# Kernel tuning notes

Measured on AMD Instinct MI355X. Metric: run time of the kernel, lower is better.

The kernel has to match this reference:

```python
import jax, jax.numpy as jnp
import numpy as np

N = 50000          # nodes
E = 1600000        # edges (avg degree 32)
G = 256            # graphs in batch
IN_DIM = 128
HID = 64
NUM_LAYERS = 12    # stacked layers after the first
NUM_REL = 3
NEG_SLOPE = 0.2    # RGATConv default leaky_relu slope


def setup_inputs() -> dict:
    key = jax.random.key(0)
    ks = jax.random.split(key, 12)
    return {
        "node_features": jax.random.normal(ks[0], (N, IN_DIM), jnp.float32),
        "edge_index": jax.random.randint(ks[1], (2, E), 0, N, jnp.int32),
        "edge_type": jax.random.randint(ks[2], (E,), 0, NUM_REL, jnp.int32),
        "batch_index": jnp.sort(jax.random.randint(ks[3], (N,), 0, G, jnp.int32)),
        "W_first": jax.random.normal(ks[4], (NUM_REL, IN_DIM, HID), jnp.float32) / np.sqrt(IN_DIM).astype(np.float32),
        "q_first": jax.random.normal(ks[5], (HID,), jnp.float32) / np.sqrt(HID).astype(np.float32),
        "k_first": jax.random.normal(ks[6], (HID,), jnp.float32) / np.sqrt(HID).astype(np.float32),
        "b_first": jnp.zeros((HID,), jnp.float32),
        "W_stack": jax.random.normal(ks[7], (NUM_LAYERS, NUM_REL, HID, HID), jnp.float32) / np.sqrt(HID).astype(np.float32),
        "q_stack": jax.random.normal(ks[8], (NUM_LAYERS, HID), jnp.float32) / np.sqrt(HID).astype(np.float32),
        "k_stack": jax.random.normal(ks[9], (NUM_LAYERS, HID), jnp.float32) / np.sqrt(HID).astype(np.float32),
        "b_stack": jnp.zeros((NUM_LAYERS, HID), jnp.float32),
        "t": jnp.ones((1,), jnp.float32),
    }


def _segment_softmax(logits, seg, num_segments):
    # numerically-stable softmax over entries sharing a segment id (PyG `softmax`)
    m = jax.ops.segment_max(logits, seg, num_segments=num_segments)
    m = jnp.where(jnp.isfinite(m), m, 0.0)  # empty segments -> -inf, neutralize
    e = jnp.exp(logits - m[seg])
    s = jax.ops.segment_sum(e, seg, num_segments=num_segments)
    return e / (s[seg] + 1e-16)


def _rgat_layer(x, W, q, k, b, src, dst, etype):
    # PyG RGATConv, heads=1, dim=1, additive-self-attention, across-relation softmax.
    n = x.shape[0]
    xr = jnp.einsum('ni,rio->rno', x, W)       # [R,N,H] per-relation transform of all nodes
    qn = jnp.einsum('rno,o->rn', xr, q)        # [R,N] query scalar (out_i @ q)
    kn = jnp.einsum('rno,o->rn', xr, k)        # [R,N] key scalar   (out_j @ k)
    logits = jax.nn.leaky_relu(qn[etype, dst] + kn[etype, src], NEG_SLOPE)  # [E]
    alpha = _segment_softmax(logits, dst, n)   # softmax over incoming edges of each dst
    msg = alpha[:, None] * xr[etype, src]      # [E,H]
    return jax.ops.segment_sum(msg, dst, num_segments=n) + b


def reference(node_features, edge_index, edge_type, batch_index,
              W_first, q_first, k_first, b_first,
              W_stack, q_stack, k_stack, b_stack, t):
    src, dst = edge_index[0], edge_index[1]   # PyG convention: row=source j, col=target i
    x1 = _rgat_layer(node_features, W_first, q_first, k_first, b_first, src, dst, edge_type)

    def step(x, p):
        W, q, k, b = p
        y = _rgat_layer(x, W, q, k, b, src, dst, edge_type)
        return y, y

    _, ys = jax.lax.scan(step, x1, (W_stack, q_stack, k_stack, b_stack))
    all_x = jnp.concatenate([x1[None], ys], axis=0)                 # [13,N,H]
    node_rep = jnp.transpose(all_x, (1, 0, 2)).reshape(node_features.shape[0], -1)  # [N,13*H]

    # SoftmaxAggregation(learn=True): per-feature softmax over nodes of each graph
    alpha_g = _segment_softmax(node_rep * t[0], batch_index, G)     # [N,13*H]
    graph_rep = jax.ops.segment_sum(node_rep * alpha_g, batch_index, num_segments=G)
    return graph_rep, node_rep
```

## Files before the change

### kernel.cpp

```cpp
#include <hip/hip_runtime.h>
#include <math.h>

#define NN 50000
#define NE 1600000
#define NG 256
#define IND 128
#define HID 64
#define NREL 3
#define SLOPE 0.2f
#define XRS 192
#define NRS 832
#define WTP 136
#define W0SZ (192*128)
#define WLSZ (192*64)
#define WTOT (W0SZ + 12*WLSZ)

typedef short bf16x8 __attribute__((ext_vector_type(8)));
typedef float f32x4 __attribute__((ext_vector_type(4)));

__device__ __forceinline__ float wred_max(float v){
  #pragma unroll
  for (int o = 32; o; o >>= 1) v = fmaxf(v, __shfl_xor(v, o));
  return v;
}
__device__ __forceinline__ float wred_sum(float v){
  #pragma unroll
  for (int o = 32; o; o >>= 1) v += __shfl_xor(v, o);
  return v;
}

__device__ __forceinline__ unsigned short f2bf(float f){
  unsigned int u = __float_as_uint(f);
  u = (u + 0x7FFFu + ((u >> 16) & 1u)) >> 16;
  return (unsigned short)u;
}
__device__ __forceinline__ float bf2f(unsigned short h){
  return __uint_as_float(((unsigned int)h) << 16);
}


__global__ void hist_kernel(const int* __restrict__ dst, int* __restrict__ cnts){
  int e = blockIdx.x * blockDim.x + threadIdx.x;
  if (e < NE) atomicAdd(&cnts[dst[e]], 1);
}

__global__ void scan1_kernel(const int* __restrict__ cnts, int* __restrict__ rowp,
                             int* __restrict__ bsum){
  __shared__ int ws[16];
  int b = blockIdx.x, tid = threadIdx.x;
  int i = b * 1024 + tid;
  int lane = tid & 63, wid = tid >> 6;
  int v = (i < NN) ? cnts[i] : 0;
  int x = v;
  #pragma unroll
  for (int o = 1; o < 64; o <<= 1){ int t = __shfl_up(x, o); if (lane >= o) x += t; }
  if (lane == 63) ws[wid] = x;
  __syncthreads();
  if (tid < 16){
    int y = ws[tid];
    #pragma unroll
    for (int o = 1; o < 16; o <<= 1){ int t = __shfl_up(y, o); if (tid >= o) y += t; }
    ws[tid] = y;
  }
  __syncthreads();
  int off = (wid > 0) ? ws[wid - 1] : 0;
  x += off;
  if (i < NN) rowp[i] = x - v;
  if (tid == 1023) bsum[b] = x;
}

__global__ void scan2_kernel(int* __restrict__ bsum, int* __restrict__ rowp, int nb){
  int tid = threadIdx.x;
  int v = (tid < nb) ? bsum[tid] : 0;
  int x = v;
  #pragma unroll
  for (int o = 1; o < 64; o <<= 1){ int t = __shfl_up(x, o); if (tid >= o) x += t; }
  if (tid < nb) bsum[tid] = x - v;
  if (tid == 63) rowp[NN] = x;
}

__global__ void scan3_kernel(int* __restrict__ rowp, const int* __restrict__ bsum){
  int i = blockIdx.x * 1024 + threadIdx.x;
  if (i < NN) rowp[i] += bsum[blockIdx.x];
}

__global__ void scatter_kernel(const int* __restrict__ src, const int* __restrict__ dst,
                               const int* __restrict__ et, const int* __restrict__ rowp,
                               int* __restrict__ fill, int* __restrict__ csr){
  int e = blockIdx.x * blockDim.x + threadIdx.x;
  if (e >= NE) return;
  int d = dst[e];
  int pos = atomicAdd(&fill[d], 1);
  csr[rowp[d] + pos] = src[e] | (et[e] << 24);
}

__global__ void gstart_kernel(const int* __restrict__ batch, int* __restrict__ gst){
  int n = blockIdx.x * blockDim.x + threadIdx.x;
  if (n > NN) return;
  int bc = (n < NN) ? batch[n] : NG;
  int bp = (n == 0) ? -1 : batch[n - 1];
  for (int g = bp + 1; g <= bc; ++g) gst[g] = n;
}

__global__ void wprep13_kernel(const float* __restrict__ Wf, const float* __restrict__ Ws,
                               unsigned short* __restrict__ Wtg13){
  int i = blockIdx.x * blockDim.x + threadIdx.x;
  if (i >= WTOT) return;
  int j, K; size_t base; const float* W;
  if (i < W0SZ){ j = i; K = IND; base = 0; W = Wf; }
  else {
    int t = i - W0SZ;
    int l = t / WLSZ;
    j = t - l * WLSZ; K = HID;
    base = W0SZ + (size_t)l * WLSZ;
    W = Ws + (size_t)l * WLSZ;
  }
  int h = j & 63;
  int k = (j >> 6) % K;
  int r = j / (K * HID);
  Wtg13[base + (size_t)((r << 6) + h) * K + k] = f2bf(W[j]);
}

__global__ __launch_bounds__(256) void mm_kernel(
    const float* __restrict__ x, int ldx, int K,
    const unsigned short* __restrict__ Wtg,
    const float* __restrict__ qv, const float* __restrict__ kv,
    unsigned short* __restrict__ XRb, float* __restrict__ QK){
  __shared__ unsigned short Wt[192 * WTP];
  int tid = threadIdx.x;
  int w = tid >> 6, lane = tid & 63;
  int lrow = lane & 15, kg = lane >> 4;
  int row0 = blockIdx.x * 64;
  int row = row0 + w * 16 + lrow;
  int nb8 = 192 * (K >> 3);
  for (int i = tid; i < nb8; i += 256){
    int col = i / (K >> 3);
    int k8 = (i - col * (K >> 3)) << 3;
    *(bf16x8*)&Wt[col * WTP + k8] = *(const bf16x8*)&Wtg[(size_t)col * K + k8];
  }
  __syncthreads();

  f32x4 acc[12];
  #pragma unroll
  for (int t = 0; t < 12; ++t) acc[t] = (f32x4){0.f, 0.f, 0.f, 0.f};

  int ksteps = K >> 5;
  for (int ks = 0; ks < ksteps; ++ks){
    bf16x8 xb;
    if (row < NN){
      const float* xp = x + (size_t)row * ldx + (ks << 5) + (kg << 3);
      float4 v0 = *(const float4*)xp;
      float4 v1 = *(const float4*)(xp + 4);
      xb[0] = (short)f2bf(v0.x); xb[1] = (short)f2bf(v0.y);
      xb[2] = (short)f2bf(v0.z); xb[3] = (short)f2bf(v0.w);
      xb[4] = (short)f2bf(v1.x); xb[5] = (short)f2bf(v1.y);
      xb[6] = (short)f2bf(v1.z); xb[7] = (short)f2bf(v1.w);
    } else {
      #pragma unroll
      for (int j = 0; j < 8; ++j) xb[j] = 0;
    }
    int kk = (ks << 5) + (kg << 3);
    #pragma unroll
    for (int t = 0; t < 12; ++t){
      bf16x8 wf = *(const bf16x8*)&Wt[(t * 16 + lrow) * WTP + kk];
      acc[t] = __builtin_amdgcn_mfma_f32_16x16x32_bf16(wf, xb, acc[t], 0, 0, 0);
    }
  }

  if (row < NN){
    unsigned short* orow = XRb + (size_t)row * XRS;
    #pragma unroll
    for (int t = 0; t < 12; ++t){
      ushort4 o4;
      o4.x = f2bf(acc[t][0]); o4.y = f2bf(acc[t][1]);
      o4.z = f2bf(acc[t][2]); o4.w = f2bf(acc[t][3]);
      *(ushort4*)(orow + t * 16 + (kg << 2)) = o4;
    }
  }

  float pq[3] = {0,0,0}, pk[3] = {0,0,0};
  #pragma unroll
  for (int t = 0; t < 12; ++t){
    int r = t >> 2;
    int hbase = ((t & 3) << 4) + (kg << 2);
    #pragma unroll
    for (int j = 0; j < 4; ++j){
      float qc = qv[hbase + j], kc = kv[hbase + j];
      pq[r] = fmaf(acc[t][j], qc, pq[r]);
      pk[r] = fmaf(acc[t][j], kc, pk[r]);
    }
  }
  #pragma unroll
  for (int o = 16; o < 64; o <<= 1){
    #pragma unroll
    for (int r = 0; r < 3; ++r){
      pq[r] += __shfl_xor(pq[r], o);
      pk[r] += __shfl_xor(pk[r], o);
    }
  }
  if (kg == 0 && row < NN){
    #pragma unroll
    for (int r = 0; r < 3; ++r){
      QK[row * 8 + r] = pq[r];
      QK[row * 8 + 3 + r] = pk[r];
    }
  }
}


__global__ __launch_bounds__(256) void edge_kernel(
    const unsigned short* __restrict__ XRb, const float* __restrict__ QK,
    const int* __restrict__ csr, const int* __restrict__ rowp,
    const float* __restrict__ bias, float* __restrict__ out){
  int wid = blockIdx.x * 4 + (threadIdx.x >> 6);
  int lane = threadIdx.x & 63;
  if (wid >= NN) return;
  int beg = rowp[wid], end = rowp[wid + 1];
  int cnt = end - beg;
  float* orow = out + (size_t)wid * NRS;
  int sub = lane & 7;
  int g   = lane >> 3;
  if (cnt == 0){
    if (lane < 8){
      float4 b0 = *(const float4*)(bias + sub * 8);
      float4 b1 = *(const float4*)(bias + sub * 8 + 4);
      *(float4*)(orow + sub * 8) = b0;
      *(float4*)(orow + sub * 8 + 4) = b1;
    }
    return;
  }
  float q0 = QK[wid * 8], q1 = QK[wid * 8 + 1], q2 = QK[wid * 8 + 2];

  if (cnt <= 128){
    float l0 = -INFINITY, l1 = -INFINITY;
    int o0 = 0, o1 = 0;
    {
      int idx = beg + lane;
      if (idx < end){
        int pk = csr[idx];
        int sn = pk & 0xFFFFFF, et = pk >> 24;
        float lg = (et == 0 ? q0 : (et == 1 ? q1 : q2)) + QK[sn * 8 + 3 + et];
        l0 = lg >= 0.f ? lg : lg * SLOPE;
        o0 = sn * XRS + et * HID;
      }
      idx += 64;
      if (idx < end){
        int pk = csr[idx];
        int sn = pk & 0xFFFFFF, et = pk >> 24;
        float lg = (et == 0 ? q0 : (et == 1 ? q1 : q2)) + QK[sn * 8 + 3 + et];
        l1 = lg >= 0.f ? lg : lg * SLOPE;
        o1 = sn * XRS + et * HID;
      }
    }
    float m = wred_max(fmaxf(l0, l1));
    float e0 = __expf(l0 - m), e1 = __expf(l1 - m);
    float s = wred_sum(e0 + e1);
    float inv = 1.f / (s + 1e-16f);
    float w0 = e0 * inv, w1 = e1 * inv;

    const unsigned short* xp = XRb + sub * 8;
    float acc[8] = {};

    float wS[8]; int oS[8];
    #pragma unroll
    for (int e = 0; e < 8; ++e){
      int sl = (e << 3) + g;
      wS[e] = __shfl(w0, sl);
      oS[e] = __shfl(o0, sl);
    }
    int nIt = (min(cnt, 64) + 7) >> 3;
    #pragma unroll
    for (int e = 0; e < 8; ++e){
      uint4 d = *(const uint4*)(xp + oS[e]);
      float we = wS[e];
      acc[0] = fmaf(we, __uint_as_float(d.x << 16), acc[0]);
      acc[1] = fmaf(we, __uint_as_float(d.x & 0xFFFF0000u), acc[1]);
      acc[2] = fmaf(we, __uint_as_float(d.y << 16), acc[2]);
      acc[3] = fmaf(we, __uint_as_float(d.y & 0xFFFF0000u), acc[3]);
      acc[4] = fmaf(we, __uint_as_float(d.z << 16), acc[4]);
      acc[5] = fmaf(we, __uint_as_float(d.z & 0xFFFF0000u), acc[5]);
      acc[6] = fmaf(we, __uint_as_float(d.w << 16), acc[6]);
      acc[7] = fmaf(we, __uint_as_float(d.w & 0xFFFF0000u), acc[7]);
      if (e + 1 >= nIt) break;
    }
    if (cnt > 64){
      #pragma unroll
      for (int e = 0; e < 8; ++e){
        int sl = (e << 3) + g;
        wS[e] = __shfl(w1, sl);
        oS[e] = __shfl(o1, sl);
      }
      int nIt2 = (cnt - 64 + 7) >> 3;
      #pragma unroll
      for (int e = 0; e < 8; ++e){
        uint4 d = *(const uint4*)(xp + oS[e]);
        float we = wS[e];
        acc[0] = fmaf(we, __uint_as_float(d.x << 16), acc[0]);
        acc[1] = fmaf(we, __uint_as_float(d.x & 0xFFFF0000u), acc[1]);
        acc[2] = fmaf(we, __uint_as_float(d.y << 16), acc[2]);
        acc[3] = fmaf(we, __uint_as_float(d.y & 0xFFFF0000u), acc[3]);
        acc[4] = fmaf(we, __uint_as_float(d.z << 16), acc[4]);
        acc[5] = fmaf(we, __uint_as_float(d.z & 0xFFFF0000u), acc[5]);
        acc[6] = fmaf(we, __uint_as_float(d.w << 16), acc[6]);
        acc[7] = fmaf(we, __uint_as_float(d.w & 0xFFFF0000u), acc[7]);
        if (e + 1 >= nIt2) break;
      }
    }
    #pragma unroll
    for (int o = 8; o < 64; o <<= 1)
      #pragma unroll
      for (int j = 0; j < 8; ++j)
        acc[j] += __shfl_xor(acc[j], o);
    if (lane < 8){
      float4 b0 = *(const float4*)(bias + sub * 8);
      float4 b1 = *(const float4*)(bias + sub * 8 + 4);
      float4 r0, r1;
      r0.x = acc[0] + b0.x; r0.y = acc[1] + b0.y; r0.z = acc[2] + b0.z; r0.w = acc[3] + b0.w;
      r1.x = acc[4] + b1.x; r1.y = acc[5] + b1.y; r1.z = acc[6] + b1.z; r1.w = acc[7] + b1.w;
      *(float4*)(orow + sub * 8) = r0;
      *(float4*)(orow + sub * 8 + 4) = r1;
    }
    return;
  }

  float bv = bias[lane];
  float m = -INFINITY, s = 0.f;
  for (int c = beg; c < end; c += 64){
    int idx = c + lane;
    float l = -INFINITY;
    if (idx < end){
      int pk = csr[idx];
      int sn = pk & 0xFFFFFF, et = pk >> 24;
      float lg = (et == 0 ? q0 : (et == 1 ? q1 : q2)) + QK[sn * 8 + 3 + et];
      l = lg >= 0.f ? lg : lg * SLOPE;
    }
    float mnew = fmaxf(m, wred_max(l));
    float ps = wred_sum((idx < end) ? __expf(l - mnew) : 0.f);
    s = s * __expf(m - mnew) + ps;
    m = mnew;
  }
  float inv = 1.f / (s + 1e-16f);
  float acc = 0.f;
  for (int c = beg; c < end; c += 64){
    int idx = c + lane;
    int off = 0; float wgt = 0.f;
    if (idx < end){
      int pk = csr[idx];
      int sn = pk & 0xFFFFFF, et = pk >> 24;
      float lg = (et == 0 ? q0 : (et == 1 ? q1 : q2)) + QK[sn * 8 + 3 + et];
      float l = lg >= 0.f ? lg : lg * SLOPE;
      wgt = __expf(l - m) * inv;
      off = sn * XRS + et * HID;
    }
    int cc = min(64, end - c);
    #pragma unroll 4
    for (int j = 0; j < cc; ++j){
      float wj = __uint_as_float(__builtin_amdgcn_readlane(__float_as_uint(wgt), j));
      int oj = __builtin_amdgcn_readlane(off, j);
      acc = fmaf(wj, bf2f(XRb[oj + lane]), acc);
    }
  }
  orow[lane] = acc + bv;
}


__global__ __launch_bounds__(256) void agg_kernel(
    const float* __restrict__ nr, const int* __restrict__ gst,
    const float* __restrict__ tp, float* __restrict__ out){
  __shared__ float rm[4][64], rs[4][64], ra[4][64];
  int g = blockIdx.x;
  int lane = threadIdx.x & 63;
  int w = threadIdx.x >> 6;
  int f = blockIdx.y * 64 + lane;
  int s = gst[g], e = gst[g + 1];
  float tval = tp[0];
  float m = -INFINITY, ss = 0.f, ac = 0.f;
  for (int n = s + w; n < e; n += 4){
    float v = nr[(size_t)n * NRS + f];
    float vm = v * tval;
    float Mn = fmaxf(m, vm);
    float sc = __expf(m - Mn);
    float ev = __expf(vm - Mn);
    ss = ss * sc + ev;
    ac = ac * sc + v * ev;
    m = Mn;
  }
  rm[w][lane] = m; rs[w][lane] = ss; ra[w][lane] = ac;
  __syncthreads();
  if (w == 0){
    float M = fmaxf(fmaxf(rm[0][lane], rm[1][lane]), fmaxf(rm[2][lane], rm[3][lane]));
    float S = 0.f, A = 0.f;
    #pragma unroll
    for (int i = 0; i < 4; ++i){
      float si = rs[i][lane];
      float sci = (si > 0.f) ? __expf(rm[i][lane] - M) : 0.f;
      S = fmaf(si, sci, S);
      A = fmaf(ra[i][lane], sci, A);
    }
    out[(size_t)g * NRS + f] = A / (S + 1e-16f);
  }
}


extern "C" void kernel_launch(void* const* d_in, const int* in_sizes, int n_in,
                              void* d_out, int out_size, void* d_ws, size_t ws_size,
                              hipStream_t stream){
  const float* x0   = (const float*)d_in[0];
  const int*   eidx = (const int*)d_in[1];
  const int*   etyp = (const int*)d_in[2];
  const int*   batch= (const int*)d_in[3];
  const float* Wf   = (const float*)d_in[4];
  const float* qf   = (const float*)d_in[5];
  const float* kf   = (const float*)d_in[6];
  const float* bf   = (const float*)d_in[7];
  const float* Ws   = (const float*)d_in[8];
  const float* qs   = (const float*)d_in[9];
  const float* ks   = (const float*)d_in[10];
  const float* bs   = (const float*)d_in[11];
  const float* tp   = (const float*)d_in[12];

  float* gout = (float*)d_out;
  float* nrep = gout + (size_t)NG * NRS;

  char* w = (char*)d_ws;
  unsigned short* XRb = (unsigned short*)w; w += (size_t)NN * XRS * 2;
  float* QK   = (float*)w;  w += (size_t)NN * 8 * 4;
  unsigned short* Wtg13 = (unsigned short*)w; w += (size_t)WTOT * 2;
  int*   rowp = (int*)w;    w += (size_t)(NN + 2) * 4;
  int*   cnts = (int*)w;    w += (size_t)NN * 4;
  int*   gst  = (int*)w;    w += (size_t)(NG + 2) * 4;
  int*   bsum = (int*)w;    w += 64 * 4;
  int*   csr  = (int*)w;    w += (size_t)NE * 4;

  const int* srcv = eidx;
  const int* dstv = eidx + NE;

  const int NB = (NN + 1023) / 1024;

  hipMemsetAsync(cnts, 0, (size_t)NN * 4, stream);
  hist_kernel<<<(NE + 255) / 256, 256, 0, stream>>>(dstv, cnts);
  scan1_kernel<<<NB, 1024, 0, stream>>>(cnts, rowp, bsum);
  scan2_kernel<<<1, 64, 0, stream>>>(bsum, rowp, NB);
  scan3_kernel<<<NB, 1024, 0, stream>>>(rowp, bsum);
  hipMemsetAsync(cnts, 0, (size_t)NN * 4, stream);
  scatter_kernel<<<(NE + 255) / 256, 256, 0, stream>>>(srcv, dstv, etyp, rowp, cnts, csr);
  gstart_kernel<<<(NN + 256) / 256, 256, 0, stream>>>(batch, gst);
  wprep13_kernel<<<(WTOT + 255) / 256, 256, 0, stream>>>(Wf, Ws, Wtg13);

  for (int l = 0; l < 13; ++l){
    int K = (l == 0) ? IND : HID;
    const unsigned short* Wtg = Wtg13 + ((l == 0) ? 0 : (W0SZ + (size_t)(l - 1) * WLSZ));
    const float* q  = (l == 0) ? qf : (qs + (size_t)(l - 1) * HID);
    const float* kv = (l == 0) ? kf : (ks + (size_t)(l - 1) * HID);
    const float* b  = (l == 0) ? bf : (bs + (size_t)(l - 1) * HID);
    const float* x  = (l == 0) ? x0 : (nrep + (size_t)(l - 1) * HID);
    int ldx = (l == 0) ? IND : NRS;
    mm_kernel<<<(NN + 63) / 64, 256, 0, stream>>>(x, ldx, K, Wtg, q, kv, XRb, QK);
    edge_kernel<<<(NN + 3) / 4, 256, 0, stream>>>(XRb, QK, csr, rowp, b, nrep + (size_t)l * HID);
  }
  dim3 ag(NG, 13);
  agg_kernel<<<ag, 256, 0, stream>>>(nrep, gst, tp, gout);
}
```

Measured before the change: 1.016 ms.

## Build CSR via two-level bucket sort with shared-memory atomics

```diff
diff --git a/kernel.cpp b/kernel.cpp
--- a/kernel.cpp
+++ b/kernel.cpp
@@ -14,6 +14,8 @@
 #define W0SZ (192*128)
 #define WLSZ (192*64)
 #define WTOT (W0SZ + 12*WLSZ)
+#define NBKT 49
+#define ACHUNK 4096
 
 typedef short bf16x8 __attribute__((ext_vector_type(8)));
 typedef float f32x4 __attribute__((ext_vector_type(4)));
@@ -39,22 +41,76 @@
 }
 
 
-__global__ void hist_kernel(const int* __restrict__ dst, int* __restrict__ cnts){
-  int e = blockIdx.x * blockDim.x + threadIdx.x;
-  if (e < NE) atomicAdd(&cnts[dst[e]], 1);
-}
-
-__global__ void scan1_kernel(const int* __restrict__ cnts, int* __restrict__ rowp,
-                             int* __restrict__ bsum){
+__global__ __launch_bounds__(256) void bhistA_kernel(const int* __restrict__ dst,
+                                                     int* __restrict__ bkt_cnt){
+  __shared__ int h[64];
+  int tid = threadIdx.x;
+  if (tid < 64) h[tid] = 0;
+  __syncthreads();
+  int e0 = blockIdx.x * ACHUNK;
+  int e1 = min(e0 + ACHUNK, NE);
+  for (int i = e0 + tid; i < e1; i += 256)
+    atomicAdd(&h[dst[i] >> 10], 1);
+  __syncthreads();
+  if (tid < 64 && h[tid] > 0) atomicAdd(&bkt_cnt[tid], h[tid]);
+}
+
+__global__ void bscan_kernel(const int* __restrict__ bkt_cnt, int* __restrict__ bkt_base,
+                             int* __restrict__ bkt_fill, int* __restrict__ rowp){
+  int tid = threadIdx.x;
+  int v = (tid < NBKT) ? bkt_cnt[tid] : 0;
+  int x = v;
+  #pragma unroll
+  for (int o = 1; o < 64; o <<= 1){ int t = __shfl_up(x, o); if (tid >= o) x += t; }
+  int excl = x - v;
+  if (tid <= NBKT){ bkt_base[tid] = excl; bkt_fill[tid] = excl; }
+  if (tid == 0) rowp[NN] = NE;
+}
+
+__global__ __launch_bounds__(256) void bscatA_kernel(
+    const int* __restrict__ src, const int* __restrict__ dst, const int* __restrict__ et,
+    int* __restrict__ bkt_fill, unsigned int* __restrict__ ebkt){
+  __shared__ int h[64];
+  __shared__ int bbase[64];
+  int tid = threadIdx.x;
+  if (tid < 64) h[tid] = 0;
+  __syncthreads();
+  int e0 = blockIdx.x * ACHUNK;
+  int e1 = min(e0 + ACHUNK, NE);
+  for (int i = e0 + tid; i < e1; i += 256)
+    atomicAdd(&h[dst[i] >> 10], 1);
+  __syncthreads();
+  if (tid < 64) bbase[tid] = (h[tid] > 0) ? atomicAdd(&bkt_fill[tid], h[tid]) : 0;
+  __syncthreads();
+  if (tid < 64) h[tid] = 0;
+  __syncthreads();
+  for (int i = e0 + tid; i < e1; i += 256){
+    int d = dst[i];
+    int b = d >> 10;
+    int pos = atomicAdd(&h[b], 1);
+    ebkt[bbase[b] + pos] =
+        ((unsigned int)(d & 1023) << 18) | ((unsigned int)(et[i] & 3) << 16) | (unsigned int)src[i];
+  }
+}
+
+__global__ __launch_bounds__(1024) void bsortB_kernel(
+    const unsigned int* __restrict__ ebkt, const int* __restrict__ bkt_base,
+    int* __restrict__ rowp, int* __restrict__ csr){
+  __shared__ int cnt[1024];
   __shared__ int ws[16];
   int b = blockIdx.x, tid = threadIdx.x;
-  int i = b * 1024 + tid;
-  int lane = tid & 63, wid = tid >> 6;
-  int v = (i < NN) ? cnts[i] : 0;
+  int beg = bkt_base[b], end = bkt_base[b + 1];
+  cnt[tid] = 0;
+  __syncthreads();
+  for (int i = beg + tid; i < end; i += 1024)
+    atomicAdd(&cnt[(ebkt[i] >> 18) & 1023], 1);
+  __syncthreads();
+  int v = cnt[tid];
+  int lane = tid & 63, wv = tid >> 6;
   int x = v;
   #pragma unroll
   for (int o = 1; o < 64; o <<= 1){ int t = __shfl_up(x, o); if (lane >= o) x += t; }
-  if (lane == 63) ws[wid] = x;
+  if (lane == 63) ws[wv] = x;
   __syncthreads();
   if (tid < 16){
     int y = ws[tid];
@@ -63,35 +119,17 @@
     ws[tid] = y;
   }
   __syncthreads();
-  int off = (wid > 0) ? ws[wid - 1] : 0;
-  x += off;
-  if (i < NN) rowp[i] = x - v;
-  if (tid == 1023) bsum[b] = x;
-}
-
-__global__ void scan2_kernel(int* __restrict__ bsum, int* __restrict__ rowp, int nb){
-  int tid = threadIdx.x;
-  int v = (tid < nb) ? bsum[tid] : 0;
-  int x = v;
-  #pragma unroll
-  for (int o = 1; o < 64; o <<= 1){ int t = __shfl_up(x, o); if (tid >= o) x += t; }
-  if (tid < nb) bsum[tid] = x - v;
-  if (tid == 63) rowp[NN] = x;
-}
-
-__global__ void scan3_kernel(int* __restrict__ rowp, const int* __restrict__ bsum){
-  int i = blockIdx.x * 1024 + threadIdx.x;
-  if (i < NN) rowp[i] += bsum[blockIdx.x];
-}
-
-__global__ void scatter_kernel(const int* __restrict__ src, const int* __restrict__ dst,
-                               const int* __restrict__ et, const int* __restrict__ rowp,
-                               int* __restrict__ fill, int* __restrict__ csr){
-  int e = blockIdx.x * blockDim.x + threadIdx.x;
-  if (e >= NE) return;
-  int d = dst[e];
-  int pos = atomicAdd(&fill[d], 1);
-  csr[rowp[d] + pos] = src[e] | (et[e] << 24);
+  int excl = x + ((wv > 0) ? ws[wv - 1] : 0) - v;
+  int node = b * 1024 + tid;
+  if (node < NN) rowp[node] = beg + excl;
+  cnt[tid] = excl;
+  __syncthreads();
+  for (int i = beg + tid; i < end; i += 1024){
+    unsigned int p = ebkt[i];
+    int dl = (p >> 18) & 1023;
+    int pos = atomicAdd(&cnt[dl], 1);
+    csr[beg + pos] = (int)(p & 0x3FFFFu);
+  }
 }
 
 __global__ void gstart_kernel(const int* __restrict__ batch, int* __restrict__ gst){
@@ -238,7 +276,7 @@
       int idx = beg + lane;
       if (idx < end){
         int pk = csr[idx];
-        int sn = pk & 0xFFFFFF, et = pk >> 24;
+        int sn = pk & 0xFFFF, et = (pk >> 16) & 3;
         float lg = (et == 0 ? q0 : (et == 1 ? q1 : q2)) + QK[sn * 8 + 3 + et];
         l0 = lg >= 0.f ? lg : lg * SLOPE;
         o0 = sn * XRS + et * HID;
@@ -246,7 +284,7 @@
       idx += 64;
       if (idx < end){
         int pk = csr[idx];
-        int sn = pk & 0xFFFFFF, et = pk >> 24;
+        int sn = pk & 0xFFFF, et = (pk >> 16) & 3;
         float lg = (et == 0 ? q0 : (et == 1 ? q1 : q2)) + QK[sn * 8 + 3 + et];
         l1 = lg >= 0.f ? lg : lg * SLOPE;
         o1 = sn * XRS + et * HID;
@@ -330,7 +368,7 @@
     float l = -INFINITY;
     if (idx < end){
       int pk = csr[idx];
-      int sn = pk & 0xFFFFFF, et = pk >> 24;
+      int sn = pk & 0xFFFF, et = (pk >> 16) & 3;
       float lg = (et == 0 ? q0 : (et == 1 ? q1 : q2)) + QK[sn * 8 + 3 + et];
       l = lg >= 0.f ? lg : lg * SLOPE;
     }
@@ -346,7 +384,7 @@
     int off = 0; float wgt = 0.f;
     if (idx < end){
       int pk = csr[idx];
-      int sn = pk & 0xFFFFFF, et = pk >> 24;
+      int sn = pk & 0xFFFF, et = (pk >> 16) & 3;
       float lg = (et == 0 ? q0 : (et == 1 ? q1 : q2)) + QK[sn * 8 + 3 + et];
       float l = lg >= 0.f ? lg : lg * SLOPE;
       wgt = __expf(l - m) * inv;
@@ -362,7 +400,6 @@
   }
   orow[lane] = acc + bv;
 }
-
 
 __global__ __launch_bounds__(256) void agg_kernel(
     const float* __restrict__ nr, const int* __restrict__ gst,
@@ -427,23 +464,23 @@
   float* QK   = (float*)w;  w += (size_t)NN * 8 * 4;
   unsigned short* Wtg13 = (unsigned short*)w; w += (size_t)WTOT * 2;
   int*   rowp = (int*)w;    w += (size_t)(NN + 2) * 4;
-  int*   cnts = (int*)w;    w += (size_t)NN * 4;
   int*   gst  = (int*)w;    w += (size_t)(NG + 2) * 4;
-  int*   bsum = (int*)w;    w += 64 * 4;
+  int*   bkt_cnt  = (int*)w; w += 64 * 4;
+  int*   bkt_base = (int*)w; w += 64 * 4;
+  int*   bkt_fill = (int*)w; w += 64 * 4;
+  unsigned int* ebkt = (unsigned int*)w; w += (size_t)NE * 4;
   int*   csr  = (int*)w;    w += (size_t)NE * 4;
 
   const int* srcv = eidx;
   const int* dstv = eidx + NE;
 
-  const int NB = (NN + 1023) / 1024;
-
-  hipMemsetAsync(cnts, 0, (size_t)NN * 4, stream);
-  hist_kernel<<<(NE + 255) / 256, 256, 0, stream>>>(dstv, cnts);
-  scan1_kernel<<<NB, 1024, 0, stream>>>(cnts, rowp, bsum);
-  scan2_kernel<<<1, 64, 0, stream>>>(bsum, rowp, NB);
-  scan3_kernel<<<NB, 1024, 0, stream>>>(rowp, bsum);
-  hipMemsetAsync(cnts, 0, (size_t)NN * 4, stream);
-  scatter_kernel<<<(NE + 255) / 256, 256, 0, stream>>>(srcv, dstv, etyp, rowp, cnts, csr);
+  const int NAB = (NE + ACHUNK - 1) / ACHUNK;
+
+  hipMemsetAsync(bkt_cnt, 0, 64 * 4, stream);
+  bhistA_kernel<<<NAB, 256, 0, stream>>>(dstv, bkt_cnt);
+  bscan_kernel<<<1, 64, 0, stream>>>(bkt_cnt, bkt_base, bkt_fill, rowp);
+  bscatA_kernel<<<NAB, 256, 0, stream>>>(srcv, dstv, etyp, bkt_fill, ebkt);
+  bsortB_kernel<<<NBKT, 1024, 0, stream>>>(ebkt, bkt_base, rowp, csr);
   gstart_kernel<<<(NN + 256) / 256, 256, 0, stream>>>(batch, gst);
   wprep13_kernel<<<(WTOT + 255) / 256, 256, 0, stream>>>(Wf, Ws, Wtg13);
 
```

Measured after the change: 903.5 us. -11.1%, faster.
